# Optimization experiments

Hardware: AMD Instinct MI355X
Metric: run time of the kernel (lower is better)

Reference implementation:

```python
import jax, jax.numpy as jnp
import numpy as np

N, L, D = 4, 2048, 1024
H_DIM, OUT_DIM = 1024, 1024


def setup_inputs() -> dict:
    key = jax.random.key(0)
    ks = jax.random.split(key, 7)
    scale = 0.02
    return {
        "x": jax.random.normal(ks[0], (N, L, D), dtype=jnp.float32),
        "Wq": jax.random.normal(ks[1], (D, H_DIM), dtype=jnp.float32) * scale,
        "bq": jnp.zeros((H_DIM,), dtype=jnp.float32),
        "Wk": jax.random.normal(ks[2], (D, H_DIM), dtype=jnp.float32) * scale,
        "bk": jnp.zeros((H_DIM,), dtype=jnp.float32),
        "Wv": jax.random.normal(ks[3], (D, OUT_DIM), dtype=jnp.float32) * scale,
        "bv": jnp.zeros((OUT_DIM,), dtype=jnp.float32),
    }


def reference(x, Wq, bq, Wk, bk, Wv, bv):
    # q,k: [N,L,h_dim], v: [N,L,out_dim]
    q = jnp.einsum("nld,dh->nlh", x, Wq) + bq
    k = jnp.einsum("nld,dh->nlh", x, Wk) + bk
    v = jnp.einsum("nld,do->nlo", x, Wv) + bv
    # scores: [N,L,L]
    qk = jnp.einsum("nlh,nmh->nlm", q, k)
    # NOTE: original scales by sqrt(qk.shape[-1]) == sqrt(L) (seq len), not sqrt(h_dim)
    seq_len = qk.shape[-1]
    s = jax.nn.softmax(qk / jnp.sqrt(jnp.asarray(seq_len, dtype=qk.dtype)), axis=-1)
    return jnp.einsum("nlm,nmo->nlo", s, v)
```

## Files before the change

### kernel.cpp

```cpp
#include <hip/hip_runtime.h>
#include <hip/hip_bf16.h>


typedef __attribute__((ext_vector_type(8))) short bf16x8;
typedef __attribute__((ext_vector_type(4))) float f32x4;

#define AS_G(p) ((__attribute__((address_space(1))) void*)(p))
#define AS_L(p) ((__attribute__((address_space(3))) void*)(p))

__device__ __forceinline__ unsigned short f2bf(float f) {
  unsigned int u = __float_as_uint(f);
  unsigned int lsb = (u >> 16) & 1u;
  u += 0x7fffu + lsb;
  return (unsigned short)(u >> 16);
}

#define WAITV(n) asm volatile("s_waitcnt vmcnt(" #n ")" ::: "memory")
#define BARRIER() do { asm volatile("" ::: "memory");                         \
    __builtin_amdgcn_s_barrier();                                             \
    asm volatile("" ::: "memory");                                            \
    __builtin_amdgcn_sched_barrier(0); } while (0)


#define S64A(ktk, rb, bofs)                                                   \
  __builtin_amdgcn_global_load_lds(                                           \
      AS_G(A + (size_t)(rowBase + (rb) * 64 + r0) * lda + (ktk) + goff),      \
      AS_L(lds + (bofs) + (rb) * 4096 + t * 8), 16, 0, 0)

#define S64B(ktk, rb, bofs)                                                   \
  __builtin_amdgcn_global_load_lds(                                           \
      AS_G(B + (size_t)(colBase + (rb) * 64 + r0) * ldb + (ktk) + goff),      \
      AS_L(lds + (bofs) + 16384 + (rb) * 4096 + t * 8), 16, 0, 0)

#define LOADA8(ih, bofs) do { _Pragma("unroll")                               \
    for (int ks_ = 0; ks_ < 2; ks_++) { _Pragma("unroll")                     \
      for (int ii = 0; ii < 4; ii++) {                                        \
        int row_ = wrow + ((ih) * 4 + ii) * 16 + r16;                         \
        int slot_ = (ks_ * 4 + q) ^ (r16 & 7);                                \
        af[ks_][ii] = *(const bf16x8*)(lds + (bofs) + row_ * 64 + slot_ * 8); \
      } } } while (0)

#define LOADA4(bofs) do { _Pragma("unroll")                                   \
    for (int ks_ = 0; ks_ < 2; ks_++) { _Pragma("unroll")                     \
      for (int ii = 0; ii < 4; ii++) {                                        \
        int row_ = wrow + ii * 16 + r16;                                      \
        int slot_ = (ks_ * 4 + q) ^ (r16 & 7);                                \
        af[ks_][ii] = *(const bf16x8*)(lds + (bofs) + row_ * 64 + slot_ * 8); \
      } } } while (0)

#define LOADB(jh, bofs) do { _Pragma("unroll")                                \
    for (int ks_ = 0; ks_ < 2; ks_++) { _Pragma("unroll")                     \
      for (int jj = 0; jj < 2; jj++) {                                        \
        int row_ = wcol + ((jh) * 2 + jj) * 16 + r16;                         \
        int slot_ = (ks_ * 4 + q) ^ (r16 & 7);                                \
        bfr[ks_][(jh) * 2 + jj] =                                             \
            *(const bf16x8*)(lds + (bofs) + 16384 + row_ * 64 + slot_ * 8);   \
      } } } while (0)

#define MMQ(ihb, j0, j1) do { __builtin_amdgcn_s_setprio(1); _Pragma("unroll")\
    for (int ks_ = 0; ks_ < 2; ks_++) { _Pragma("unroll")                     \
      for (int ii = 0; ii < 4; ii++) { _Pragma("unroll")                      \
        for (int jj = (j0); jj <= (j1); jj++)                                 \
          acc[(ihb) + ii][jj] = __builtin_amdgcn_mfma_f32_16x16x32_bf16(      \
              af[ks_][ii], bfr[ks_][jj], acc[(ihb) + ii][jj], 0, 0, 0);       \
      } }                                                                     \
    __builtin_amdgcn_s_setprio(0); } while (0)

#define TILE8(ktc, bofs, obofs) do {                                          \
    LOADA8(0, bofs); LOADB(0, bofs); LOADB(1, bofs);                          \
    if ((ktc) && (ktc) + 64 < K) {                                            \
      S64A((ktc) + 64, 1, obofs); S64A((ktc) + 64, 3, obofs);                 \
    }                                                                         \
    MMQ(0, 0, 3);                                                             \
    BARRIER();                                                                \
    LOADA8(1, bofs);                                                          \
    if ((ktc) + 128 < K) {                                                    \
      S64A((ktc) + 128, 0, bofs); S64A((ktc) + 128, 2, bofs);                 \
      S64B((ktc) + 128, 0, bofs); S64B((ktc) + 128, 1, bofs);                 \
      S64B((ktc) + 128, 2, bofs); S64B((ktc) + 128, 3, bofs);                 \
    }                                                                         \
    MMQ(4, 0, 3);                                                             \
    if ((ktc) + 128 < K) { WAITV(6); } else { WAITV(0); }                     \
    BARRIER(); } while (0)

#define TILE4(ktc, bofs, obofs) do {                                          \
    LOADA4(bofs); LOADB(0, bofs);                                             \
    if ((ktc) && (ktc) + 64 < K) {                                            \
      S64B((ktc) + 64, 0, obofs); S64B((ktc) + 64, 1, obofs);                 \
    }                                                                         \
    MMQ(0, 0, 1);                                                             \
    BARRIER();                                                                \
    LOADB(1, bofs);                                                           \
    if ((ktc) + 128 < K) {                                                    \
      S64A((ktc) + 128, 0, bofs); S64A((ktc) + 128, 1, bofs);                 \
      S64A((ktc) + 128, 2, bofs); S64A((ktc) + 128, 3, bofs);                 \
    }                                                                         \
    MMQ(0, 2, 3);                                                             \
    if ((ktc) + 128 < K) { WAITV(4); } else { WAITV(0); }                     \
    BARRIER(); } while (0)

template <int EPI, int MI>
__global__ __launch_bounds__(512, 2) void gemm_2r(
    const unsigned short* __restrict__ A, const unsigned short* __restrict__ B,
    float* __restrict__ Cf, long long sA, long long sB, long long sC,
    int K, int lda, int ldb, int ldc,
    unsigned short* __restrict__ u0, unsigned short* __restrict__ u1,
    unsigned short* __restrict__ u2,
    const float* __restrict__ f0, const float* __restrict__ f1,
    const float* __restrict__ f2,
    float* __restrict__ rsum, float scale)
{
  constexpr int BN = MI * 32;
  constexpr int BUFE = 16384 + BN * 64;
  __shared__ unsigned short lds[2 * BUFE];

  const int t = threadIdx.x;
  const int rowBase = blockIdx.y * 256;
  const int colBase = blockIdx.x * BN;
  A += (long long)blockIdx.z * sA;
  B += (long long)blockIdx.z * sB;

  const int l = t & 63;
  const int w = t >> 6;
  const int wrow = (MI == 8) ? (w >> 2) * 128 : (w >> 1) * 64;
  const int wcol = (MI == 8) ? (w & 3) * 64 : (w & 1) * 64;
  const int q = l >> 4;
  const int r16 = l & 15;

  const int r0 = t >> 3;
  const int goff = ((t & 7) ^ (r0 & 7)) << 3;

  f32x4 acc[MI][4] = {};
  bf16x8 af[2][4], bfr[2][4];

  S64A(0, 0, 0); S64A(0, 1, 0); S64A(0, 2, 0); S64A(0, 3, 0);
  S64B(0, 0, 0); S64B(0, 1, 0);
  if constexpr (MI == 8) { S64B(0, 2, 0); S64B(0, 3, 0); }
  S64A(64, 0, BUFE); S64A(64, 1, BUFE); S64A(64, 2, BUFE); S64A(64, 3, BUFE);
  S64B(64, 0, BUFE); S64B(64, 1, BUFE);
  if constexpr (MI == 8) { S64B(64, 2, BUFE); S64B(64, 3, BUFE); }
  if constexpr (MI == 8) { WAITV(8); } else { WAITV(6); }
  BARRIER();

  for (int kt = 0; kt < K; kt += 128) {
    if constexpr (MI == 8) {
      TILE8(kt, 0, BUFE);
      TILE8(kt + 64, BUFE, 0);
    } else {
      TILE4(kt, 0, BUFE);
      TILE4(kt + 64, BUFE, 0);
    }
  }

  if (EPI == 1) {
    unsigned short* p16 = u0 + (long long)blockIdx.z * sC;
    float* rs = rsum + (long long)blockIdx.z * 2048;
#pragma unroll
    for (int i = 0; i < MI; i++) {
#pragma unroll
      for (int r = 0; r < 4; r++) {
        int row = rowBase + wrow + i * 16 + q * 4 + r;
        float rowpart = 0.f;
#pragma unroll
        for (int j = 0; j < 4; j++) {
          int col = colBase + wcol + j * 16 + r16;
          float e = __expf(acc[i][j][r] * scale);
          p16[(size_t)row * ldc + col] = f2bf(e);
          rowpart += e;
        }
#pragma unroll
        for (int m = 1; m < 16; m <<= 1) rowpart += __shfl_xor(rowpart, m);
        if (r16 == 0) atomicAdd(rs + row, rowpart);
      }
    }
  } else if (EPI == 2) {
    const int seg = colBase >> 10;
    if (seg < 2) {
      unsigned short* dst = seg ? u1 : u0;
      const float* bias = seg ? f1 : f0;
      const int cb = colBase & 1023;
#pragma unroll
      for (int i = 0; i < MI; i++) {
#pragma unroll
        for (int r = 0; r < 4; r++) {
          int row = rowBase + wrow + i * 16 + q * 4 + r;
#pragma unroll
          for (int j = 0; j < 4; j++) {
            int col = cb + wcol + j * 16 + r16;
            dst[(size_t)row * 1024 + col] = f2bf(acc[i][j][r] + bias[col]);
          }
        }
      }
    } else {
      const int ob = colBase - 2048;
#pragma unroll
      for (int i = 0; i < MI; i++) {
        int posBase = rowBase + wrow + i * 16 + q * 4;
        int b = posBase >> 11;
        int pos = posBase & 2047;
#pragma unroll
        for (int j = 0; j < 4; j++) {
          int o = ob + wcol + j * 16 + r16;
          float bias = f2[o];
          ushort4 pk;
          pk.x = f2bf(acc[i][j][0] + bias);
          pk.y = f2bf(acc[i][j][1] + bias);
          pk.z = f2bf(acc[i][j][2] + bias);
          pk.w = f2bf(acc[i][j][3] + bias);
          *(ushort4*)(u2 + ((size_t)((b << 10) + o) * 2048 + pos)) = pk;
        }
      }
    }
  } else {
    float* C = Cf + (long long)blockIdx.z * sC;
    const float* rs = rsum + (long long)blockIdx.z * 2048;
#pragma unroll
    for (int i = 0; i < MI; i++) {
#pragma unroll
      for (int r = 0; r < 4; r++) {
        int row = rowBase + wrow + i * 16 + q * 4 + r;
        float inv = 1.0f / rs[row];
#pragma unroll
        for (int j = 0; j < 4; j++) {
          int col = colBase + wcol + j * 16 + r16;
          C[(size_t)row * ldc + col] = acc[i][j][r] * inv;
        }
      }
    }
  }
}


__global__ __launch_bounds__(256) void cast_f32_to_bf16(
    const float* __restrict__ in, unsigned short* __restrict__ out, int n4,
    float* __restrict__ rzero, int nz4)
{
  int i = blockIdx.x * 256 + threadIdx.x;
  if (i < nz4) ((float4*)rzero)[i] = make_float4(0.f, 0.f, 0.f, 0.f);
  if (i >= n4) return;
  float4 v = ((const float4*)in)[i];
  ushort4 o;
  o.x = f2bf(v.x); o.y = f2bf(v.y); o.z = f2bf(v.z); o.w = f2bf(v.w);
  ((ushort4*)out)[i] = o;
}


__global__ __launch_bounds__(256) void wtrans(
    const float* __restrict__ Wq, const float* __restrict__ Wk,
    const float* __restrict__ Wv, unsigned short* __restrict__ WT)
{
  __shared__ float tile[32][33];
  const float* in = blockIdx.z == 0 ? Wq : (blockIdx.z == 1 ? Wk : Wv);
  unsigned short* out = WT + (size_t)blockIdx.z * 1024 * 1024;
  const int bc = blockIdx.x * 32;
  const int br = blockIdx.y * 32;
  const int tx = threadIdx.x;
  const int ty = threadIdx.y;
#pragma unroll
  for (int i = 0; i < 4; i++)
    tile[ty + i * 8][tx] = in[(size_t)(br + ty + i * 8) * 1024 + bc + tx];
  __syncthreads();
#pragma unroll
  for (int i = 0; i < 4; i++)
    out[(size_t)(bc + ty + i * 8) * 1024 + br + tx] = f2bf(tile[tx][ty + i * 8]);
}


extern "C" void kernel_launch(void* const* d_in, const int* in_sizes, int n_in,
                              void* d_out, int out_size, void* d_ws, size_t ws_size,
                              hipStream_t stream) {
  (void)in_sizes; (void)n_in; (void)out_size;

  const float* x  = (const float*)d_in[0];
  const float* Wq = (const float*)d_in[1];
  const float* bq = (const float*)d_in[2];
  const float* Wk = (const float*)d_in[3];
  const float* bk = (const float*)d_in[4];
  const float* Wv = (const float*)d_in[5];
  const float* bv = (const float*)d_in[6];
  float* out = (float*)d_out;

  const int Nb = 4, L = 2048, D = 1024, H = 1024, O = 1024;
  const int M = Nb * L;
  const int NQKV = 3 * H;

  char* ws = (char*)d_ws;
  size_t off = 0;
  unsigned short* xb = (unsigned short*)(ws + off); off += (size_t)M * D * 2;
  unsigned short* qb = (unsigned short*)(ws + off); off += (size_t)M * H * 2;
  unsigned short* kb = (unsigned short*)(ws + off); off += (size_t)M * H * 2;
  unsigned short* vt = (unsigned short*)(ws + off); off += (size_t)M * O * 2;
  unsigned short* WT = (unsigned short*)(ws + off); off += (size_t)NQKV * D * 2;
  unsigned short* P  = (unsigned short*)(ws + off); off += (size_t)Nb * L * L * 2;
  float* rsum = (float*)(ws + off); off += (size_t)Nb * L * 4;
  if (ws_size < off) return;

  dim3 blk256(256);
  dim3 blk512(512);

  cast_f32_to_bf16<<<(M * D / 4 + 255) / 256, blk256, 0, stream>>>(
      x, xb, M * D / 4, rsum, Nb * L / 4);

  wtrans<<<dim3(32, 32, 3), dim3(32, 8), 0, stream>>>(Wq, Wk, Wv, WT);

  gemm_2r<2, 4><<<dim3(NQKV / 128, M / 256, 1), blk512, 0, stream>>>(
      xb, WT, nullptr, 0, 0, 0, D, D, D, 0,
      qb, kb, vt, bq, bk, bv, nullptr, 0.f);

  gemm_2r<1, 8><<<dim3(L / 256, L / 256, Nb), blk512, 0, stream>>>(
      qb, kb, nullptr, (long long)L * H, (long long)L * H, (long long)L * L,
      H, H, H, L,
      P, nullptr, nullptr, nullptr, nullptr, nullptr,
      rsum, 0.022097086912079608f );

  gemm_2r<3, 4><<<dim3(O / 128, L / 256, Nb), blk512, 0, stream>>>(
      P, vt, out, (long long)L * L, (long long)O * L, (long long)L * O,
      L, L, L, O,
      nullptr, nullptr, nullptr, nullptr, nullptr, nullptr,
      rsum, 0.f);
}
```

Before: 247.8 us.

## Launch exactly 256 blocks with multiple column tiles per block for QKV and scores

Adds a TILES template parameter so each workgroup loops over several output column tiles, and launches the QKV projection and score GEMMs with 256 blocks (one per CU on MI355X). The score GEMM also switches from 256x256 tiles (MI=8) to 256x128 tiles (MI=4) with two tiles per block. The aim is to remove partial-wave tail effects and give balanced per-CU work. In exchange, each block runs its tiles serially with a pipeline refill between them, and the smaller score tiles give less operand reuse.

```diff
diff --git a/kernel.cpp b/kernel.cpp
--- a/kernel.cpp
+++ b/kernel.cpp
@@ -99,7 +99,7 @@
     if ((ktc) + 128 < K) { WAITV(4); } else { WAITV(0); }                     \
     BARRIER(); } while (0)
 
-template <int EPI, int MI>
+template <int EPI, int MI, int TILES>
 __global__ __launch_bounds__(512, 2) void gemm_2r(
     const unsigned short* __restrict__ A, const unsigned short* __restrict__ B,
     float* __restrict__ Cf, long long sA, long long sB, long long sC,
@@ -115,10 +115,22 @@
   __shared__ unsigned short lds[2 * BUFE];
 
   const int t = threadIdx.x;
-  const int rowBase = blockIdx.y * 256;
-  const int colBase = blockIdx.x * BN;
-  A += (long long)blockIdx.z * sA;
-  B += (long long)blockIdx.z * sB;
+
+  int tx0, tyy, tzz;
+  if constexpr (TILES == 1) {
+    tx0 = blockIdx.x; tyy = blockIdx.y; tzz = blockIdx.z;
+  } else if constexpr (TILES == 2) {
+    tzz = blockIdx.x >> 6;
+    tyy = (blockIdx.x & 63) >> 3;
+    tx0 = blockIdx.x & 7;
+  } else {
+    tzz = 0;
+    tyy = blockIdx.x >> 3;
+    tx0 = blockIdx.x & 7;
+  }
+  const int rowBase = tyy * 256;
+  A += (long long)tzz * sA;
+  B += (long long)tzz * sB;
 
   const int l = t & 63;
   const int w = t >> 6;
@@ -130,100 +142,105 @@
   const int r0 = t >> 3;
   const int goff = ((t & 7) ^ (r0 & 7)) << 3;
 
-  f32x4 acc[MI][4] = {};
-  bf16x8 af[2][4], bfr[2][4];
-
-  S64A(0, 0, 0); S64A(0, 1, 0); S64A(0, 2, 0); S64A(0, 3, 0);
-  S64B(0, 0, 0); S64B(0, 1, 0);
-  if constexpr (MI == 8) { S64B(0, 2, 0); S64B(0, 3, 0); }
-  S64A(64, 0, BUFE); S64A(64, 1, BUFE); S64A(64, 2, BUFE); S64A(64, 3, BUFE);
-  S64B(64, 0, BUFE); S64B(64, 1, BUFE);
-  if constexpr (MI == 8) { S64B(64, 2, BUFE); S64B(64, 3, BUFE); }
-  if constexpr (MI == 8) { WAITV(8); } else { WAITV(6); }
-  BARRIER();
-
-  for (int kt = 0; kt < K; kt += 128) {
-    if constexpr (MI == 8) {
-      TILE8(kt, 0, BUFE);
-      TILE8(kt + 64, BUFE, 0);
-    } else {
-      TILE4(kt, 0, BUFE);
-      TILE4(kt + 64, BUFE, 0);
-    }
-  }
-
-  if (EPI == 1) {
-    unsigned short* p16 = u0 + (long long)blockIdx.z * sC;
-    float* rs = rsum + (long long)blockIdx.z * 2048;
-#pragma unroll
-    for (int i = 0; i < MI; i++) {
-#pragma unroll
-      for (int r = 0; r < 4; r++) {
-        int row = rowBase + wrow + i * 16 + q * 4 + r;
-        float rowpart = 0.f;
-#pragma unroll
-        for (int j = 0; j < 4; j++) {
-          int col = colBase + wcol + j * 16 + r16;
-          float e = __expf(acc[i][j][r] * scale);
-          p16[(size_t)row * ldc + col] = f2bf(e);
-          rowpart += e;
-        }
-#pragma unroll
-        for (int m = 1; m < 16; m <<= 1) rowpart += __shfl_xor(rowpart, m);
-        if (r16 == 0) atomicAdd(rs + row, rowpart);
+#pragma unroll 1
+  for (int itile = 0; itile < TILES; ++itile) {
+    const int colBase = (tx0 + 8 * itile) * BN;
+
+    f32x4 acc[MI][4] = {};
+    bf16x8 af[2][4], bfr[2][4];
+
+    S64A(0, 0, 0); S64A(0, 1, 0); S64A(0, 2, 0); S64A(0, 3, 0);
+    S64B(0, 0, 0); S64B(0, 1, 0);
+    if constexpr (MI == 8) { S64B(0, 2, 0); S64B(0, 3, 0); }
+    S64A(64, 0, BUFE); S64A(64, 1, BUFE); S64A(64, 2, BUFE); S64A(64, 3, BUFE);
+    S64B(64, 0, BUFE); S64B(64, 1, BUFE);
+    if constexpr (MI == 8) { S64B(64, 2, BUFE); S64B(64, 3, BUFE); }
+    if constexpr (MI == 8) { WAITV(8); } else { WAITV(6); }
+    BARRIER();
+
+    for (int kt = 0; kt < K; kt += 128) {
+      if constexpr (MI == 8) {
+        TILE8(kt, 0, BUFE);
+        TILE8(kt + 64, BUFE, 0);
+      } else {
+        TILE4(kt, 0, BUFE);
+        TILE4(kt + 64, BUFE, 0);
       }
     }
-  } else if (EPI == 2) {
-    const int seg = colBase >> 10;
-    if (seg < 2) {
-      unsigned short* dst = seg ? u1 : u0;
-      const float* bias = seg ? f1 : f0;
-      const int cb = colBase & 1023;
+
+    if (EPI == 1) {
+      unsigned short* p16 = u0 + (long long)tzz * sC;
+      float* rs = rsum + (long long)tzz * 2048;
 #pragma unroll
       for (int i = 0; i < MI; i++) {
 #pragma unroll
         for (int r = 0; r < 4; r++) {
           int row = rowBase + wrow + i * 16 + q * 4 + r;
+          float rowpart = 0.f;
 #pragma unroll
           for (int j = 0; j < 4; j++) {
-            int col = cb + wcol + j * 16 + r16;
-            dst[(size_t)row * 1024 + col] = f2bf(acc[i][j][r] + bias[col]);
+            int col = colBase + wcol + j * 16 + r16;
+            float e = __expf(acc[i][j][r] * scale);
+            p16[(size_t)row * ldc + col] = f2bf(e);
+            rowpart += e;
+          }
+#pragma unroll
+          for (int m = 1; m < 16; m <<= 1) rowpart += __shfl_xor(rowpart, m);
+          if (r16 == 0) atomicAdd(rs + row, rowpart);
+        }
+      }
+    } else if (EPI == 2) {
+      const int seg = colBase >> 10;
+      if (seg < 2) {
+        unsigned short* dst = seg ? u1 : u0;
+        const float* bias = seg ? f1 : f0;
+        const int cb = colBase & 1023;
+#pragma unroll
+        for (int i = 0; i < MI; i++) {
+#pragma unroll
+          for (int r = 0; r < 4; r++) {
+            int row = rowBase + wrow + i * 16 + q * 4 + r;
+#pragma unroll
+            for (int j = 0; j < 4; j++) {
+              int col = cb + wcol + j * 16 + r16;
+              dst[(size_t)row * 1024 + col] = f2bf(acc[i][j][r] + bias[col]);
+            }
+          }
+        }
+      } else {
+        const int ob = colBase - 2048;
+#pragma unroll
+        for (int i = 0; i < MI; i++) {
+          int posBase = rowBase + wrow + i * 16 + q * 4;
+          int b = posBase >> 11;
+          int pos = posBase & 2047;
+#pragma unroll
+          for (int j = 0; j < 4; j++) {
+            int o = ob + wcol + j * 16 + r16;
+            float bias = f2[o];
+            ushort4 pk;
+            pk.x = f2bf(acc[i][j][0] + bias);
+            pk.y = f2bf(acc[i][j][1] + bias);
+            pk.z = f2bf(acc[i][j][2] + bias);
+            pk.w = f2bf(acc[i][j][3] + bias);
+            *(ushort4*)(u2 + ((size_t)((b << 10) + o) * 2048 + pos)) = pk;
           }
         }
       }
     } else {
-      const int ob = colBase - 2048;
+      float* C = Cf + (long long)tzz * sC;
+      const float* rs = rsum + (long long)tzz * 2048;
 #pragma unroll
       for (int i = 0; i < MI; i++) {
-        int posBase = rowBase + wrow + i * 16 + q * 4;
-        int b = posBase >> 11;
-        int pos = posBase & 2047;
-#pragma unroll
-        for (int j = 0; j < 4; j++) {
-          int o = ob + wcol + j * 16 + r16;
-          float bias = f2[o];
-          ushort4 pk;
-          pk.x = f2bf(acc[i][j][0] + bias);
-          pk.y = f2bf(acc[i][j][1] + bias);
-          pk.z = f2bf(acc[i][j][2] + bias);
-          pk.w = f2bf(acc[i][j][3] + bias);
-          *(ushort4*)(u2 + ((size_t)((b << 10) + o) * 2048 + pos)) = pk;
-        }
-      }
-    }
-  } else {
-    float* C = Cf + (long long)blockIdx.z * sC;
-    const float* rs = rsum + (long long)blockIdx.z * 2048;
-#pragma unroll
-    for (int i = 0; i < MI; i++) {
-#pragma unroll
-      for (int r = 0; r < 4; r++) {
-        int row = rowBase + wrow + i * 16 + q * 4 + r;
-        float inv = 1.0f / rs[row];
-#pragma unroll
-        for (int j = 0; j < 4; j++) {
-          int col = colBase + wcol + j * 16 + r16;
-          C[(size_t)row * ldc + col] = acc[i][j][r] * inv;
+#pragma unroll
+        for (int r = 0; r < 4; r++) {
+          int row = rowBase + wrow + i * 16 + q * 4 + r;
+          float inv = 1.0f / rs[row];
+#pragma unroll
+          for (int j = 0; j < 4; j++) {
+            int col = colBase + wcol + j * 16 + r16;
+            C[(size_t)row * ldc + col] = acc[i][j][r] * inv;
+          }
         }
       }
     }
@@ -303,17 +320,17 @@
 
   wtrans<<<dim3(32, 32, 3), dim3(32, 8), 0, stream>>>(Wq, Wk, Wv, WT);
 
-  gemm_2r<2, 4><<<dim3(NQKV / 128, M / 256, 1), blk512, 0, stream>>>(
+  gemm_2r<2, 4, 3><<<dim3(256), blk512, 0, stream>>>(
       xb, WT, nullptr, 0, 0, 0, D, D, D, 0,
       qb, kb, vt, bq, bk, bv, nullptr, 0.f);
 
-  gemm_2r<1, 8><<<dim3(L / 256, L / 256, Nb), blk512, 0, stream>>>(
+  gemm_2r<1, 4, 2><<<dim3(256), blk512, 0, stream>>>(
       qb, kb, nullptr, (long long)L * H, (long long)L * H, (long long)L * L,
       H, H, H, L,
       P, nullptr, nullptr, nullptr, nullptr, nullptr,
       rsum, 0.022097086912079608f );
 
-  gemm_2r<3, 4><<<dim3(O / 128, L / 256, Nb), blk512, 0, stream>>>(
+  gemm_2r<3, 4, 1><<<dim3(O / 128, L / 256, Nb), blk512, 0, stream>>>(
       P, vt, out, (long long)L * L, (long long)O * L, (long long)L * O,
       L, L, L, O,
       nullptr, nullptr, nullptr, nullptr, nullptr, nullptr,
```

Result: slower. 266.4 us (+7.5%).
